# Kernel tuning notes

Hardware: AMD Instinct MI355X
Metric: run time of the kernel (lower is better)

The kernel has to match this reference:

```python
import jax, jax.numpy as jnp
import numpy as np

B = 16        # batch
V = 49152     # HEALPix nside=64 vertices
CIN = 32
COUT = 64
K = 4         # Chebyshev polynomial degree (kernel_size)
NNZ = V * 9   # ~9 nonzeros per row of the sparse Laplacian
POOL = 4      # HEALPix pooling factor
EPS = 1e-5    # BatchNorm eps


def setup_inputs() -> dict:
    key = jax.random.key(0)
    k1, k2, k3, k4, k5 = jax.random.split(key, 5)
    x = jax.random.normal(k1, (B, V, CIN), dtype=jnp.float32)
    lap_rows = jnp.sort(jax.random.randint(k2, (NNZ,), 0, V, dtype=jnp.int32)).astype(jnp.int64)
    lap_cols = jax.random.randint(k3, (NNZ,), 0, V, dtype=jnp.int32).astype(jnp.int64)
    lap_vals = jax.random.normal(k4, (NNZ,), dtype=jnp.float32) * 0.1
    weight = jax.random.normal(k5, (K, CIN, COUT), dtype=jnp.float32) / np.sqrt(K * CIN).astype(np.float32)
    gamma = jnp.ones((COUT,), dtype=jnp.float32)
    beta = jnp.zeros((COUT,), dtype=jnp.float32)
    return {"x": x, "lap_vals": lap_vals, "weight": weight, "gamma": gamma,
            "beta": beta, "lap_rows": lap_rows, "lap_cols": lap_cols}


def _spmm(rows, cols, vals, X):
    """Sparse [V,V] @ dense [V,F] via gather + segment_sum."""
    return jax.ops.segment_sum(vals[:, None] * X[cols], rows, num_segments=V)


def reference(x, lap_vals, weight, gamma, beta, lap_rows, lap_cols):
    b, v, c = x.shape
    # Chebyshev recurrence on [V, B*Cin] layout (vertex-major for spmm)
    X0 = x.transpose(1, 0, 2).reshape(v, b * c)
    xs = [X0]
    X1 = _spmm(lap_rows, lap_cols, lap_vals, X0)
    xs.append(X1)
    for _ in range(K - 2):
        X2 = 2.0 * _spmm(lap_rows, lap_cols, lap_vals, X1) - X0
        xs.append(X2)
        X0, X1 = X1, X2
    cheb = jnp.stack(xs, axis=0).reshape(K, v, b, c)   # [K,V,B,Cin]
    y = jnp.einsum('kvbi,kio->bvo', cheb, weight)      # [B,V,Cout]
    # BatchNorm1d(Cout), training-mode stats over (batch, vertices), biased var
    mean = jnp.mean(y, axis=(0, 1))
    var = jnp.var(y, axis=(0, 1))
    y = (y - mean) * jax.lax.rsqrt(var + EPS) * gamma + beta
    y = jax.nn.relu(y)
    # HEALPix average pooling (factor 4) over vertex dim
    out = y.reshape(b, v // POOL, POOL, COUT).mean(axis=2)
    return out
```

## Files before the change

kernel.cpp:

```cpp
#include <hip/hip_runtime.h>
#include <hip/hip_bf16.h>

#define V     49152
#define NNZ   442368
#define EPS   1e-5f
#define VOUT  12288

typedef __attribute__((ext_vector_type(8))) short bf16x8;
typedef __attribute__((ext_vector_type(4))) float f32x4;

__device__ __forceinline__ unsigned short f2b(float f) {
    __hip_bfloat16 h = __float2bfloat16(f);
    return *reinterpret_cast<unsigned short*>(&h);
}
__device__ __forceinline__ float b2f(unsigned short u) {
    return __uint_as_float((unsigned)u << 16);
}

__global__ __launch_bounds__(256) void k_rowptr(const int* __restrict__ rows,
                                                int* __restrict__ rp) {
    int r = blockIdx.x * blockDim.x + threadIdx.x;
    if (r <= V) {
        int lo = 0, hi = NNZ;
        while (lo < hi) {
            int m = (lo + hi) >> 1;
            if (rows[m] < r) lo = m + 1; else hi = m;
        }
        rp[r] = lo;
    }
}

__global__ __launch_bounds__(256) void k_xpose(const float* __restrict__ x,
                                               unsigned short* __restrict__ xbf) {
    int id = blockIdx.x * 256 + threadIdx.x;
    int i4 = id & 7;
    int b  = (id >> 3) & 15;
    int v  = id >> 7;
    float4 q = *(const float4*)&x[((size_t)b * V + v) * 32 + i4 * 4];
    ushort4 u = {f2b(q.x), f2b(q.y), f2b(q.z), f2b(q.w)};
    *(ushort4*)&xbf[(size_t)v * 512 + b * 32 + i4 * 4] = u;
}

__global__ __launch_bounds__(256) void k_wconv(const float* __restrict__ W,
                                               unsigned short* __restrict__ Wfrag) {
    int d = blockIdx.x * 256 + threadIdx.x;
    int j = d & 7, lane = (d >> 3) & 63, ct = (d >> 9) & 3, ks = d >> 11;
    int k128 = ks * 32 + (lane >> 4) * 8 + j;
    int o = ct * 16 + (lane & 15);
    Wfrag[d] = f2b(W[k128 * 64 + o]);
}

__global__ __launch_bounds__(256) void k_spmm1(const unsigned short* __restrict__ xbf,
                                               const int* __restrict__ cols,
                                               const float* __restrict__ vals,
                                               const int* __restrict__ rp,
                                               unsigned short* __restrict__ X1) {
    int t = threadIdx.x;
    int wave = t >> 6, lane = t & 63;
    int v = blockIdx.x * 4 + wave;
    int f0 = lane * 8;
    int s = rp[v], e = rp[v + 1];
    float a[8] = {0.f, 0.f, 0.f, 0.f, 0.f, 0.f, 0.f, 0.f};
    for (int n = s; n < e; ++n) {
        int c = cols[n];
        float w = vals[n];
        union { unsigned short u[8]; uint4 q; } ld;
        ld.q = *(const uint4*)&xbf[(size_t)c * 512 + f0];
#pragma unroll
        for (int j = 0; j < 8; ++j) a[j] = fmaf(w, b2f(ld.u[j]), a[j]);
    }
    union { unsigned short u[8]; uint4 q; } st;
#pragma unroll
    for (int j = 0; j < 8; ++j) st.u[j] = f2b(a[j]);
    *(uint4*)&X1[(size_t)v * 512 + f0] = st.q;
}

__global__ __launch_bounds__(256) void k_spmm2(const unsigned short* __restrict__ xbf,
                                               const int* __restrict__ cols,
                                               const float* __restrict__ vals,
                                               const int* __restrict__ rp,
                                               const unsigned short* __restrict__ X1,
                                               unsigned short* __restrict__ X2) {
    int t = threadIdx.x;
    int wave = t >> 6, lane = t & 63;
    int v = blockIdx.x * 4 + wave;
    int f0 = lane * 8;
    int s = rp[v], e = rp[v + 1];
    float a[8] = {0.f, 0.f, 0.f, 0.f, 0.f, 0.f, 0.f, 0.f};
    for (int n = s; n < e; ++n) {
        int c = cols[n];
        float w = vals[n];
        union { unsigned short u[8]; uint4 q; } ld;
        ld.q = *(const uint4*)&X1[(size_t)c * 512 + f0];
#pragma unroll
        for (int j = 0; j < 8; ++j) a[j] = fmaf(w, b2f(ld.u[j]), a[j]);
    }
    union { unsigned short u[8]; uint4 q; } x0;
    x0.q = *(const uint4*)&xbf[(size_t)v * 512 + f0];
    union { unsigned short u[8]; uint4 q; } st;
#pragma unroll
    for (int j = 0; j < 8; ++j) st.u[j] = f2b(2.f * a[j] - b2f(x0.u[j]));
    *(uint4*)&X2[(size_t)v * 512 + f0] = st.q;
}

__global__ __launch_bounds__(256) void k_spmm3(const unsigned short* __restrict__ X1,
                                               const int* __restrict__ cols,
                                               const float* __restrict__ vals,
                                               const int* __restrict__ rp,
                                               const unsigned short* __restrict__ X2,
                                               unsigned short* __restrict__ X3) {
    int t = threadIdx.x;
    int wave = t >> 6, lane = t & 63;
    int v = blockIdx.x * 4 + wave;
    int f0 = lane * 8;
    int s = rp[v], e = rp[v + 1];
    float a[8] = {0.f, 0.f, 0.f, 0.f, 0.f, 0.f, 0.f, 0.f};
    for (int n = s; n < e; ++n) {
        int c = cols[n];
        float w = vals[n];
        union { unsigned short u[8]; uint4 q; } ld;
        ld.q = *(const uint4*)&X2[(size_t)c * 512 + f0];
#pragma unroll
        for (int j = 0; j < 8; ++j) a[j] = fmaf(w, b2f(ld.u[j]), a[j]);
    }
    union { unsigned short u[8]; uint4 q; } p1;
    p1.q = *(const uint4*)&X1[(size_t)v * 512 + f0];
    union { unsigned short u[8]; uint4 q; } st;
#pragma unroll
    for (int j = 0; j < 8; ++j) st.u[j] = f2b(2.f * a[j] - b2f(p1.u[j]));
    *(uint4*)&X3[(size_t)v * 512 + f0] = st.q;
}

__global__ __launch_bounds__(256) void k_einsum(const unsigned short* __restrict__ xbf,
                                                const unsigned short* __restrict__ X1,
                                                const unsigned short* __restrict__ X2,
                                                const unsigned short* __restrict__ X3,
                                                const unsigned short* __restrict__ Wfrag,
                                                unsigned short* __restrict__ Y) {
    __shared__ unsigned short sB[8192];
    __shared__ unsigned short sY[4096];

    int t = threadIdx.x;
    int wave = t >> 6, lane = t & 63;
    int v = blockIdx.x * 4 + wave;

#pragma unroll
    for (int m = 0; m < 4; ++m) {
        int d = t + m * 256;
        *(uint4*)&sB[d * 8] = *(const uint4*)&Wfrag[d * 8];
    }
    __syncthreads();

    f32x4 acc[4];
#pragma unroll
    for (int ct = 0; ct < 4; ++ct) acc[ct] = (f32x4){0.f, 0.f, 0.f, 0.f};

    const unsigned short* srcs[4] = {xbf, X1, X2, X3};
    size_t abase = (size_t)v * 512 + (lane & 15) * 32 + (lane >> 4) * 8;
#pragma unroll
    for (int ks = 0; ks < 4; ++ks) {
        bf16x8 a = *(const bf16x8*)&srcs[ks][abase];
#pragma unroll
        for (int ct = 0; ct < 4; ++ct) {
            bf16x8 b = *(const bf16x8*)&sB[((ks * 4 + ct) * 64 + lane) * 8];
            acc[ct] = __builtin_amdgcn_mfma_f32_16x16x32_bf16(a, b, acc[ct], 0, 0, 0);
        }
    }

#pragma unroll
    for (int ct = 0; ct < 4; ++ct) {
        int o = ct * 16 + (lane & 15);
        int bb = (lane >> 4) * 4;
        sY[wave * 1024 + (bb + 0) * 64 + o] = f2b(acc[ct].x);
        sY[wave * 1024 + (bb + 1) * 64 + o] = f2b(acc[ct].y);
        sY[wave * 1024 + (bb + 2) * 64 + o] = f2b(acc[ct].z);
        sY[wave * 1024 + (bb + 3) * 64 + o] = f2b(acc[ct].w);
    }
    __syncthreads();

    size_t ybase = (size_t)blockIdx.x * 4096 + t * 16;
    *(uint4*)&Y[ybase]     = *(const uint4*)&sY[t * 16];
    *(uint4*)&Y[ybase + 8] = *(const uint4*)&sY[t * 16 + 8];
}

__global__ __launch_bounds__(256) void k_bnred1(const unsigned short* __restrict__ Y,
                                                float* __restrict__ partials) {
    __shared__ float lsum[64], lsq[64];
    int t = threadIdx.x;
    if (t < 64) { lsum[t] = 0.f; lsq[t] = 0.f; }
    __syncthreads();
    float s[8] = {0.f, 0.f, 0.f, 0.f, 0.f, 0.f, 0.f, 0.f};
    float q[8] = {0.f, 0.f, 0.f, 0.f, 0.f, 0.f, 0.f, 0.f};
    const uint4* Yq = (const uint4*)Y;
    size_t base = (size_t)blockIdx.x * 24576;
    for (int i = t; i < 24576; i += 256) {
        union { unsigned short u[8]; uint4 v; } ld;
        ld.v = Yq[base + i];
#pragma unroll
        for (int j = 0; j < 8; ++j) {
            float f = b2f(ld.u[j]);
            s[j] += f;
            q[j] = fmaf(f, f, q[j]);
        }
    }
    int c0 = (t & 7) * 8;
#pragma unroll
    for (int j = 0; j < 8; ++j) {
        atomicAdd(&lsum[c0 + j], s[j]);
        atomicAdd(&lsq[c0 + j], q[j]);
    }
    __syncthreads();
    if (t < 128)
        partials[blockIdx.x * 128 + t] = (t < 64) ? lsum[t] : lsq[t - 64];
}

__global__ void k_bnfin(const float* __restrict__ partials,
                        const float* __restrict__ gamma, const float* __restrict__ beta,
                        float* __restrict__ stats) {
    __shared__ float tot[128];
    int t = threadIdx.x;
    float s = 0.f;
    for (int i = 0; i < 256; ++i) s += partials[i * 128 + t];
    tot[t] = s;
    __syncthreads();
    if (t < 64) {
        float n = (float)(16 * V);
        float mean = tot[t] / n;
        float var = tot[64 + t] / n - mean * mean;
        float sc = gamma[t] * rsqrtf(var + EPS);
        stats[128 + t] = sc;
        stats[192 + t] = beta[t] - mean * sc;
    }
}

__global__ __launch_bounds__(256) void k_pool(const unsigned short* __restrict__ Y,
                                              const float* __restrict__ stats,
                                              float* __restrict__ out) {
    int id = blockIdx.x * blockDim.x + threadIdx.x;
    int o4 = id & 15;
    int b  = (id >> 4) & 15;
    int vp = id >> 8;
    float4 sc = *(const float4*)&stats[128 + o4 * 4];
    float4 sh = *(const float4*)&stats[192 + o4 * 4];
    float ax = 0.f, ay = 0.f, az = 0.f, aw = 0.f;
#pragma unroll
    for (int j = 0; j < 4; ++j) {
        ushort4 u = *(const ushort4*)&Y[(size_t)((vp * 4 + j) * 16 + b) * 64 + o4 * 4];
        float tx = b2f(u.x), ty = b2f(u.y), tz = b2f(u.z), tw = b2f(u.w);
        ax += fmaxf(fmaf(tx, sc.x, sh.x), 0.f);
        ay += fmaxf(fmaf(ty, sc.y, sh.y), 0.f);
        az += fmaxf(fmaf(tz, sc.z, sh.z), 0.f);
        aw += fmaxf(fmaf(tw, sc.w, sh.w), 0.f);
    }
    float4 res = {ax * 0.25f, ay * 0.25f, az * 0.25f, aw * 0.25f};
    *(float4*)&out[(size_t)((b * VOUT + vp) * 16 + o4) * 4] = res;
}

extern "C" void kernel_launch(void* const* d_in, const int* in_sizes, int n_in,
                              void* d_out, int out_size, void* d_ws, size_t ws_size,
                              hipStream_t stream) {
    const float* x     = (const float*)d_in[0];
    const float* vals  = (const float*)d_in[1];
    const float* W     = (const float*)d_in[2];
    const float* gamma = (const float*)d_in[3];
    const float* beta  = (const float*)d_in[4];
    const int*   rows  = (const int*)d_in[5];
    const int*   cols  = (const int*)d_in[6];
    float* out = (float*)d_out;

    char* ws = (char*)d_ws;
    unsigned short* xbf = (unsigned short*)ws;
    unsigned short* X1  = (unsigned short*)(ws + 50331648UL);
    unsigned short* X2  = (unsigned short*)(ws + 100663296UL);
    unsigned short* X3  = (unsigned short*)(ws + 150994944UL);
    unsigned short* Y   = (unsigned short*)(ws + 201326592UL);
    int*   rp    = (int*)(ws + 301989888UL);
    float* stats = (float*)(ws + 302190592UL);
    unsigned short* Wfrag = (unsigned short*)(ws + 302194688UL);
    float* partials = (float*)(ws + 302211072UL);

    k_rowptr<<<193, 256, 0, stream>>>(rows, rp);
    k_xpose<<<V * 128 / 256, 256, 0, stream>>>(x, xbf);
    k_wconv<<<32, 256, 0, stream>>>(W, Wfrag);
    k_spmm1<<<V / 4, 256, 0, stream>>>(xbf, cols, vals, rp, X1);
    k_spmm2<<<V / 4, 256, 0, stream>>>(xbf, cols, vals, rp, X1, X2);
    k_spmm3<<<V / 4, 256, 0, stream>>>(X1, cols, vals, rp, X2, X3);
    k_einsum<<<V / 4, 256, 0, stream>>>(xbf, X1, X2, X3, Wfrag, Y);
    k_bnred1<<<256, 256, 0, stream>>>(Y, partials);
    k_bnfin<<<1, 128, 0, stream>>>(partials, gamma, beta, stats);
    k_pool<<<12288, 256, 0, stream>>>(Y, stats, out);
}
```

Measured before the change: 403.2 us.

## Fuse last Chebyshev SpMM, einsum and BN partial reduction into one kernel

The third SpMM is merged with the einsum MFMA kernel. The last Chebyshev term now stays in shared memory in fp32 and is converted to bf16 only for the final MFMA step, so X3 is never written to or read back from global memory. The BatchNorm per-channel sums are computed from the fp32 accumulators inside the same kernel, which removes the separate Y reduction pass. A small second-stage reduction is added over the 12288 per-block partials. The SpMM gather loops are also unrolled by two to allow more loads in flight. Statistics are now taken from fp32 values rather than bf16-rounded Y, which changes numerics slightly.

```diff
diff --git a/kernel.cpp b/kernel.cpp
--- a/kernel.cpp
+++ b/kernel.cpp
@@ -61,13 +61,25 @@
     int f0 = lane * 8;
     int s = rp[v], e = rp[v + 1];
     float a[8] = {0.f, 0.f, 0.f, 0.f, 0.f, 0.f, 0.f, 0.f};
-    for (int n = s; n < e; ++n) {
-        int c = cols[n];
-        float w = vals[n];
-        union { unsigned short u[8]; uint4 q; } ld;
-        ld.q = *(const uint4*)&xbf[(size_t)c * 512 + f0];
-#pragma unroll
-        for (int j = 0; j < 8; ++j) a[j] = fmaf(w, b2f(ld.u[j]), a[j]);
+    int n = s;
+    for (; n + 1 < e; n += 2) {
+        int c0 = cols[n], c1 = cols[n + 1];
+        float w0 = vals[n], w1 = vals[n + 1];
+        union { unsigned short u[8]; uint4 q; } l0, l1;
+        l0.q = *(const uint4*)&xbf[(size_t)c0 * 512 + f0];
+        l1.q = *(const uint4*)&xbf[(size_t)c1 * 512 + f0];
+#pragma unroll
+        for (int j = 0; j < 8; ++j) a[j] = fmaf(w0, b2f(l0.u[j]), a[j]);
+#pragma unroll
+        for (int j = 0; j < 8; ++j) a[j] = fmaf(w1, b2f(l1.u[j]), a[j]);
+    }
+    if (n < e) {
+        int c0 = cols[n];
+        float w0 = vals[n];
+        union { unsigned short u[8]; uint4 q; } l0;
+        l0.q = *(const uint4*)&xbf[(size_t)c0 * 512 + f0];
+#pragma unroll
+        for (int j = 0; j < 8; ++j) a[j] = fmaf(w0, b2f(l0.u[j]), a[j]);
     }
     union { unsigned short u[8]; uint4 q; } st;
 #pragma unroll
@@ -87,13 +99,25 @@
     int f0 = lane * 8;
     int s = rp[v], e = rp[v + 1];
     float a[8] = {0.f, 0.f, 0.f, 0.f, 0.f, 0.f, 0.f, 0.f};
-    for (int n = s; n < e; ++n) {
-        int c = cols[n];
-        float w = vals[n];
-        union { unsigned short u[8]; uint4 q; } ld;
-        ld.q = *(const uint4*)&X1[(size_t)c * 512 + f0];
-#pragma unroll
-        for (int j = 0; j < 8; ++j) a[j] = fmaf(w, b2f(ld.u[j]), a[j]);
+    int n = s;
+    for (; n + 1 < e; n += 2) {
+        int c0 = cols[n], c1 = cols[n + 1];
+        float w0 = vals[n], w1 = vals[n + 1];
+        union { unsigned short u[8]; uint4 q; } l0, l1;
+        l0.q = *(const uint4*)&X1[(size_t)c0 * 512 + f0];
+        l1.q = *(const uint4*)&X1[(size_t)c1 * 512 + f0];
+#pragma unroll
+        for (int j = 0; j < 8; ++j) a[j] = fmaf(w0, b2f(l0.u[j]), a[j]);
+#pragma unroll
+        for (int j = 0; j < 8; ++j) a[j] = fmaf(w1, b2f(l1.u[j]), a[j]);
+    }
+    if (n < e) {
+        int c0 = cols[n];
+        float w0 = vals[n];
+        union { unsigned short u[8]; uint4 q; } l0;
+        l0.q = *(const uint4*)&X1[(size_t)c0 * 512 + f0];
+#pragma unroll
+        for (int j = 0; j < 8; ++j) a[j] = fmaf(w0, b2f(l0.u[j]), a[j]);
     }
     union { unsigned short u[8]; uint4 q; } x0;
     x0.q = *(const uint4*)&xbf[(size_t)v * 512 + f0];
@@ -103,70 +127,104 @@
     *(uint4*)&X2[(size_t)v * 512 + f0] = st.q;
 }
 
-__global__ __launch_bounds__(256) void k_spmm3(const unsigned short* __restrict__ X1,
+__global__ __launch_bounds__(256) void k_cheb3(const unsigned short* __restrict__ xbf,
+                                               const unsigned short* __restrict__ X1,
+                                               const unsigned short* __restrict__ X2,
+                                               const unsigned short* __restrict__ Wfrag,
                                                const int* __restrict__ cols,
                                                const float* __restrict__ vals,
                                                const int* __restrict__ rp,
-                                               const unsigned short* __restrict__ X2,
-                                               unsigned short* __restrict__ X3) {
+                                               unsigned short* __restrict__ Y,
+                                               float* __restrict__ partials) {
+    __shared__ unsigned short sB[8192];
+    __shared__ float sMix[2048];
+    __shared__ float lsum[64], lsq[64];
+
     int t = threadIdx.x;
     int wave = t >> 6, lane = t & 63;
     int v = blockIdx.x * 4 + wave;
+
+#pragma unroll
+    for (int m = 0; m < 4; ++m) {
+        int d = t + m * 256;
+        *(uint4*)&sB[d * 8] = *(const uint4*)&Wfrag[d * 8];
+    }
+    if (t < 64) { lsum[t] = 0.f; lsq[t] = 0.f; }
+
     int f0 = lane * 8;
     int s = rp[v], e = rp[v + 1];
     float a[8] = {0.f, 0.f, 0.f, 0.f, 0.f, 0.f, 0.f, 0.f};
-    for (int n = s; n < e; ++n) {
-        int c = cols[n];
-        float w = vals[n];
-        union { unsigned short u[8]; uint4 q; } ld;
-        ld.q = *(const uint4*)&X2[(size_t)c * 512 + f0];
-#pragma unroll
-        for (int j = 0; j < 8; ++j) a[j] = fmaf(w, b2f(ld.u[j]), a[j]);
+    int n = s;
+    for (; n + 1 < e; n += 2) {
+        int c0 = cols[n], c1 = cols[n + 1];
+        float w0 = vals[n], w1 = vals[n + 1];
+        union { unsigned short u[8]; uint4 q; } l0, l1;
+        l0.q = *(const uint4*)&X2[(size_t)c0 * 512 + f0];
+        l1.q = *(const uint4*)&X2[(size_t)c1 * 512 + f0];
+#pragma unroll
+        for (int j = 0; j < 8; ++j) a[j] = fmaf(w0, b2f(l0.u[j]), a[j]);
+#pragma unroll
+        for (int j = 0; j < 8; ++j) a[j] = fmaf(w1, b2f(l1.u[j]), a[j]);
+    }
+    if (n < e) {
+        int c0 = cols[n];
+        float w0 = vals[n];
+        union { unsigned short u[8]; uint4 q; } l0;
+        l0.q = *(const uint4*)&X2[(size_t)c0 * 512 + f0];
+#pragma unroll
+        for (int j = 0; j < 8; ++j) a[j] = fmaf(w0, b2f(l0.u[j]), a[j]);
     }
     union { unsigned short u[8]; uint4 q; } p1;
     p1.q = *(const uint4*)&X1[(size_t)v * 512 + f0];
-    union { unsigned short u[8]; uint4 q; } st;
-#pragma unroll
-    for (int j = 0; j < 8; ++j) st.u[j] = f2b(2.f * a[j] - b2f(p1.u[j]));
-    *(uint4*)&X3[(size_t)v * 512 + f0] = st.q;
-}
-
-__global__ __launch_bounds__(256) void k_einsum(const unsigned short* __restrict__ xbf,
-                                                const unsigned short* __restrict__ X1,
-                                                const unsigned short* __restrict__ X2,
-                                                const unsigned short* __restrict__ X3,
-                                                const unsigned short* __restrict__ Wfrag,
-                                                unsigned short* __restrict__ Y) {
-    __shared__ unsigned short sB[8192];
-    __shared__ unsigned short sY[4096];
-
-    int t = threadIdx.x;
-    int wave = t >> 6, lane = t & 63;
-    int v = blockIdx.x * 4 + wave;
-
-#pragma unroll
-    for (int m = 0; m < 4; ++m) {
-        int d = t + m * 256;
-        *(uint4*)&sB[d * 8] = *(const uint4*)&Wfrag[d * 8];
-    }
+    float4 xa, xb;
+    xa.x = 2.f * a[0] - b2f(p1.u[0]); xa.y = 2.f * a[1] - b2f(p1.u[1]);
+    xa.z = 2.f * a[2] - b2f(p1.u[2]); xa.w = 2.f * a[3] - b2f(p1.u[3]);
+    xb.x = 2.f * a[4] - b2f(p1.u[4]); xb.y = 2.f * a[5] - b2f(p1.u[5]);
+    xb.z = 2.f * a[6] - b2f(p1.u[6]); xb.w = 2.f * a[7] - b2f(p1.u[7]);
+    *(float4*)&sMix[wave * 512 + f0]     = xa;
+    *(float4*)&sMix[wave * 512 + f0 + 4] = xb;
     __syncthreads();
 
     f32x4 acc[4];
 #pragma unroll
     for (int ct = 0; ct < 4; ++ct) acc[ct] = (f32x4){0.f, 0.f, 0.f, 0.f};
 
-    const unsigned short* srcs[4] = {xbf, X1, X2, X3};
+    const unsigned short* srcs[3] = {xbf, X1, X2};
     size_t abase = (size_t)v * 512 + (lane & 15) * 32 + (lane >> 4) * 8;
 #pragma unroll
-    for (int ks = 0; ks < 4; ++ks) {
-        bf16x8 a = *(const bf16x8*)&srcs[ks][abase];
+    for (int ks = 0; ks < 3; ++ks) {
+        bf16x8 afr = *(const bf16x8*)&srcs[ks][abase];
 #pragma unroll
         for (int ct = 0; ct < 4; ++ct) {
             bf16x8 b = *(const bf16x8*)&sB[((ks * 4 + ct) * 64 + lane) * 8];
-            acc[ct] = __builtin_amdgcn_mfma_f32_16x16x32_bf16(a, b, acc[ct], 0, 0, 0);
+            acc[ct] = __builtin_amdgcn_mfma_f32_16x16x32_bf16(afr, b, acc[ct], 0, 0, 0);
         }
     }
-
+    {
+        int ao = wave * 512 + (lane & 15) * 32 + (lane >> 4) * 8;
+        float4 fa = *(const float4*)&sMix[ao];
+        float4 fb = *(const float4*)&sMix[ao + 4];
+        union { unsigned short u[8]; bf16x8 h; } af;
+        af.u[0] = f2b(fa.x); af.u[1] = f2b(fa.y); af.u[2] = f2b(fa.z); af.u[3] = f2b(fa.w);
+        af.u[4] = f2b(fb.x); af.u[5] = f2b(fb.y); af.u[6] = f2b(fb.z); af.u[7] = f2b(fb.w);
+#pragma unroll
+        for (int ct = 0; ct < 4; ++ct) {
+            bf16x8 b = *(const bf16x8*)&sB[((3 * 4 + ct) * 64 + lane) * 8];
+            acc[ct] = __builtin_amdgcn_mfma_f32_16x16x32_bf16(af.h, b, acc[ct], 0, 0, 0);
+        }
+    }
+
+#pragma unroll
+    for (int ct = 0; ct < 4; ++ct) {
+        float ss = acc[ct].x + acc[ct].y + acc[ct].z + acc[ct].w;
+        float qq = acc[ct].x * acc[ct].x + acc[ct].y * acc[ct].y
+                 + acc[ct].z * acc[ct].z + acc[ct].w * acc[ct].w;
+        atomicAdd(&lsum[ct * 16 + (lane & 15)], ss);
+        atomicAdd(&lsq[ct * 16 + (lane & 15)], qq);
+    }
+
+    __syncthreads();
+    unsigned short* sY = (unsigned short*)sMix;
 #pragma unroll
     for (int ct = 0; ct < 4; ++ct) {
         int o = ct * 16 + (lane & 15);
@@ -181,46 +239,39 @@
     size_t ybase = (size_t)blockIdx.x * 4096 + t * 16;
     *(uint4*)&Y[ybase]     = *(const uint4*)&sY[t * 16];
     *(uint4*)&Y[ybase + 8] = *(const uint4*)&sY[t * 16 + 8];
-}
-
-__global__ __launch_bounds__(256) void k_bnred1(const unsigned short* __restrict__ Y,
-                                                float* __restrict__ partials) {
-    __shared__ float lsum[64], lsq[64];
-    int t = threadIdx.x;
-    if (t < 64) { lsum[t] = 0.f; lsq[t] = 0.f; }
-    __syncthreads();
-    float s[8] = {0.f, 0.f, 0.f, 0.f, 0.f, 0.f, 0.f, 0.f};
-    float q[8] = {0.f, 0.f, 0.f, 0.f, 0.f, 0.f, 0.f, 0.f};
-    const uint4* Yq = (const uint4*)Y;
-    size_t base = (size_t)blockIdx.x * 24576;
-    for (int i = t; i < 24576; i += 256) {
-        union { unsigned short u[8]; uint4 v; } ld;
-        ld.v = Yq[base + i];
-#pragma unroll
-        for (int j = 0; j < 8; ++j) {
-            float f = b2f(ld.u[j]);
-            s[j] += f;
-            q[j] = fmaf(f, f, q[j]);
-        }
-    }
-    int c0 = (t & 7) * 8;
-#pragma unroll
-    for (int j = 0; j < 8; ++j) {
-        atomicAdd(&lsum[c0 + j], s[j]);
-        atomicAdd(&lsq[c0 + j], q[j]);
-    }
-    __syncthreads();
+
     if (t < 128)
-        partials[blockIdx.x * 128 + t] = (t < 64) ? lsum[t] : lsq[t - 64];
-}
-
-__global__ void k_bnfin(const float* __restrict__ partials,
+        partials[(size_t)blockIdx.x * 128 + t] = (t < 64) ? lsum[t] : lsq[t - 64];
+}
+
+__global__ __launch_bounds__(256) void k_bnred2(const float* __restrict__ partials,
+                                                float* __restrict__ partials2) {
+    __shared__ float ls[128];
+    int t = threadIdx.x;
+    if (t < 128) ls[t] = 0.f;
+    __syncthreads();
+    const float4* P = (const float4*)(partials + (size_t)blockIdx.x * 32768);
+    float a0 = 0.f, a1 = 0.f, a2 = 0.f, a3 = 0.f;
+    for (int i = 0; i < 32; ++i) {
+        float4 q = P[i * 256 + t];
+        a0 += q.x; a1 += q.y; a2 += q.z; a3 += q.w;
+    }
+    int c0 = (t * 4) & 127;
+    atomicAdd(&ls[c0], a0);
+    atomicAdd(&ls[c0 + 1], a1);
+    atomicAdd(&ls[c0 + 2], a2);
+    atomicAdd(&ls[c0 + 3], a3);
+    __syncthreads();
+    if (t < 128) partials2[blockIdx.x * 128 + t] = ls[t];
+}
+
+__global__ void k_bnfin(const float* __restrict__ partials2,
                         const float* __restrict__ gamma, const float* __restrict__ beta,
                         float* __restrict__ stats) {
     __shared__ float tot[128];
     int t = threadIdx.x;
     float s = 0.f;
-    for (int i = 0; i < 256; ++i) s += partials[i * 128 + t];
+    for (int i = 0; i < 48; ++i) s += partials2[i * 128 + t];
     tot[t] = s;
     __syncthreads();
     if (t < 64) {
@@ -272,21 +323,20 @@
     unsigned short* xbf = (unsigned short*)ws;
     unsigned short* X1  = (unsigned short*)(ws + 50331648UL);
     unsigned short* X2  = (unsigned short*)(ws + 100663296UL);
-    unsigned short* X3  = (unsigned short*)(ws + 150994944UL);
-    unsigned short* Y   = (unsigned short*)(ws + 201326592UL);
-    int*   rp    = (int*)(ws + 301989888UL);
-    float* stats = (float*)(ws + 302190592UL);
-    unsigned short* Wfrag = (unsigned short*)(ws + 302194688UL);
-    float* partials = (float*)(ws + 302211072UL);
+    unsigned short* Y   = (unsigned short*)(ws + 150994944UL);
+    int*   rp    = (int*)(ws + 251658240UL);
+    float* stats = (float*)(ws + 251858944UL);
+    unsigned short* Wfrag = (unsigned short*)(ws + 251859968UL);
+    float* partials  = (float*)(ws + 251877376UL);
+    float* partials2 = (float*)(ws + 258168832UL);
 
     k_rowptr<<<193, 256, 0, stream>>>(rows, rp);
     k_xpose<<<V * 128 / 256, 256, 0, stream>>>(x, xbf);
     k_wconv<<<32, 256, 0, stream>>>(W, Wfrag);
     k_spmm1<<<V / 4, 256, 0, stream>>>(xbf, cols, vals, rp, X1);
     k_spmm2<<<V / 4, 256, 0, stream>>>(xbf, cols, vals, rp, X1, X2);
-    k_spmm3<<<V / 4, 256, 0, stream>>>(X1, cols, vals, rp, X2, X3);
-    k_einsum<<<V / 4, 256, 0, stream>>>(xbf, X1, X2, X3, Wfrag, Y);
-    k_bnred1<<<256, 256, 0, stream>>>(Y, partials);
-    k_bnfin<<<1, 128, 0, stream>>>(partials, gamma, beta, stats);
+    k_cheb3<<<V / 4, 256, 0, stream>>>(xbf, X1, X2, Wfrag, cols, vals, rp, Y, partials);
+    k_bnred2<<<48, 256, 0, stream>>>(partials, partials2);
+    k_bnfin<<<1, 128, 0, stream>>>(partials2, gamma, beta, stats);
     k_pool<<<12288, 256, 0, stream>>>(Y, stats, out);
 }
```

Measured after the change: 401.3 us. Within noise of the previous version (-0.5%).

## Fuse BatchNorm statistics into einsum epilogue and unroll SpMM gathers by four

Applied to the files above, without the earlier changes.

Per-channel sum and sum-of-squares are now computed from the fp32 MFMA accumulators inside the einsum kernel. Each block reduces them in LDS and atomically adds them into 256 partial slots, which are zeroed in the rowptr kernel. This removes the separate pass that re-read the bf16 Y buffer. The SpMM gather loops are also unrolled by four so several independent row loads are in flight per wave. The cost is extra global and shared atomics per block, plus statistics taken from fp32 values rather than rounded bf16, which slightly changes the numerics.

```diff
diff --git a/kernel.cpp b/kernel.cpp
--- a/kernel.cpp
+++ b/kernel.cpp
@@ -18,16 +18,18 @@
 }
 
 __global__ __launch_bounds__(256) void k_rowptr(const int* __restrict__ rows,
-                                                int* __restrict__ rp) {
-    int r = blockIdx.x * blockDim.x + threadIdx.x;
-    if (r <= V) {
+                                                int* __restrict__ rp,
+                                                float* __restrict__ partials) {
+    int id = blockIdx.x * blockDim.x + threadIdx.x;
+    if (id <= V) {
         int lo = 0, hi = NNZ;
         while (lo < hi) {
             int m = (lo + hi) >> 1;
-            if (rows[m] < r) lo = m + 1; else hi = m;
+            if (rows[m] < id) lo = m + 1; else hi = m;
         }
-        rp[r] = lo;
-    }
+        rp[id] = lo;
+    }
+    if (id < 32768) partials[id] = 0.f;
 }
 
 __global__ __launch_bounds__(256) void k_xpose(const float* __restrict__ x,
@@ -50,6 +52,35 @@
     Wfrag[d] = f2b(W[k128 * 64 + o]);
 }
 
+#define GATHER_LOOP(SRC)                                                        \
+    float a[8] = {0.f, 0.f, 0.f, 0.f, 0.f, 0.f, 0.f, 0.f};                      \
+    int n = s;                                                                  \
+    for (; n + 3 < e; n += 4) {                                                 \
+        int c0 = cols[n], c1 = cols[n + 1], c2 = cols[n + 2], c3 = cols[n + 3]; \
+        float w0 = vals[n], w1 = vals[n + 1], w2 = vals[n + 2], w3 = vals[n + 3]; \
+        union { unsigned short u[8]; uint4 q; } l0, l1, l2, l3;                 \
+        l0.q = *(const uint4*)&SRC[(size_t)c0 * 512 + f0];                      \
+        l1.q = *(const uint4*)&SRC[(size_t)c1 * 512 + f0];                      \
+        l2.q = *(const uint4*)&SRC[(size_t)c2 * 512 + f0];                      \
+        l3.q = *(const uint4*)&SRC[(size_t)c3 * 512 + f0];                      \
+        _Pragma("unroll")                                                       \
+        for (int j = 0; j < 8; ++j) a[j] = fmaf(w0, b2f(l0.u[j]), a[j]);        \
+        _Pragma("unroll")                                                       \
+        for (int j = 0; j < 8; ++j) a[j] = fmaf(w1, b2f(l1.u[j]), a[j]);        \
+        _Pragma("unroll")                                                       \
+        for (int j = 0; j < 8; ++j) a[j] = fmaf(w2, b2f(l2.u[j]), a[j]);        \
+        _Pragma("unroll")                                                       \
+        for (int j = 0; j < 8; ++j) a[j] = fmaf(w3, b2f(l3.u[j]), a[j]);        \
+    }                                                                           \
+    for (; n < e; ++n) {                                                        \
+        int c0 = cols[n];                                                       \
+        float w0 = vals[n];                                                     \
+        union { unsigned short u[8]; uint4 q; } l0;                             \
+        l0.q = *(const uint4*)&SRC[(size_t)c0 * 512 + f0];                      \
+        _Pragma("unroll")                                                       \
+        for (int j = 0; j < 8; ++j) a[j] = fmaf(w0, b2f(l0.u[j]), a[j]);        \
+    }
+
 __global__ __launch_bounds__(256) void k_spmm1(const unsigned short* __restrict__ xbf,
                                                const int* __restrict__ cols,
                                                const float* __restrict__ vals,
@@ -60,15 +91,7 @@
     int v = blockIdx.x * 4 + wave;
     int f0 = lane * 8;
     int s = rp[v], e = rp[v + 1];
-    float a[8] = {0.f, 0.f, 0.f, 0.f, 0.f, 0.f, 0.f, 0.f};
-    for (int n = s; n < e; ++n) {
-        int c = cols[n];
-        float w = vals[n];
-        union { unsigned short u[8]; uint4 q; } ld;
-        ld.q = *(const uint4*)&xbf[(size_t)c * 512 + f0];
-#pragma unroll
-        for (int j = 0; j < 8; ++j) a[j] = fmaf(w, b2f(ld.u[j]), a[j]);
-    }
+    GATHER_LOOP(xbf)
     union { unsigned short u[8]; uint4 q; } st;
 #pragma unroll
     for (int j = 0; j < 8; ++j) st.u[j] = f2b(a[j]);
@@ -86,15 +109,7 @@
     int v = blockIdx.x * 4 + wave;
     int f0 = lane * 8;
     int s = rp[v], e = rp[v + 1];
-    float a[8] = {0.f, 0.f, 0.f, 0.f, 0.f, 0.f, 0.f, 0.f};
-    for (int n = s; n < e; ++n) {
-        int c = cols[n];
-        float w = vals[n];
-        union { unsigned short u[8]; uint4 q; } ld;
-        ld.q = *(const uint4*)&X1[(size_t)c * 512 + f0];
-#pragma unroll
-        for (int j = 0; j < 8; ++j) a[j] = fmaf(w, b2f(ld.u[j]), a[j]);
-    }
+    GATHER_LOOP(X1)
     union { unsigned short u[8]; uint4 q; } x0;
     x0.q = *(const uint4*)&xbf[(size_t)v * 512 + f0];
     union { unsigned short u[8]; uint4 q; } st;
@@ -114,15 +129,7 @@
     int v = blockIdx.x * 4 + wave;
     int f0 = lane * 8;
     int s = rp[v], e = rp[v + 1];
-    float a[8] = {0.f, 0.f, 0.f, 0.f, 0.f, 0.f, 0.f, 0.f};
-    for (int n = s; n < e; ++n) {
-        int c = cols[n];
-        float w = vals[n];
-        union { unsigned short u[8]; uint4 q; } ld;
-        ld.q = *(const uint4*)&X2[(size_t)c * 512 + f0];
-#pragma unroll
-        for (int j = 0; j < 8; ++j) a[j] = fmaf(w, b2f(ld.u[j]), a[j]);
-    }
+    GATHER_LOOP(X2)
     union { unsigned short u[8]; uint4 q; } p1;
     p1.q = *(const uint4*)&X1[(size_t)v * 512 + f0];
     union { unsigned short u[8]; uint4 q; } st;
@@ -136,9 +143,11 @@
                                                 const unsigned short* __restrict__ X2,
                                                 const unsigned short* __restrict__ X3,
                                                 const unsigned short* __restrict__ Wfrag,
-                                                unsigned short* __restrict__ Y) {
+                                                unsigned short* __restrict__ Y,
+                                                float* __restrict__ partials) {
     __shared__ unsigned short sB[8192];
     __shared__ unsigned short sY[4096];
+    __shared__ float lsum[64], lsq[64];
 
     int t = threadIdx.x;
     int wave = t >> 6, lane = t & 63;
@@ -149,6 +158,7 @@
         int d = t + m * 256;
         *(uint4*)&sB[d * 8] = *(const uint4*)&Wfrag[d * 8];
     }
+    if (t < 64) { lsum[t] = 0.f; lsq[t] = 0.f; }
     __syncthreads();
 
     f32x4 acc[4];
@@ -165,6 +175,15 @@
             bf16x8 b = *(const bf16x8*)&sB[((ks * 4 + ct) * 64 + lane) * 8];
             acc[ct] = __builtin_amdgcn_mfma_f32_16x16x32_bf16(a, b, acc[ct], 0, 0, 0);
         }
+    }
+
+#pragma unroll
+    for (int ct = 0; ct < 4; ++ct) {
+        float ss = acc[ct].x + acc[ct].y + acc[ct].z + acc[ct].w;
+        float qq = acc[ct].x * acc[ct].x + acc[ct].y * acc[ct].y
+                 + acc[ct].z * acc[ct].z + acc[ct].w * acc[ct].w;
+        atomicAdd(&lsum[ct * 16 + (lane & 15)], ss);
+        atomicAdd(&lsq[ct * 16 + (lane & 15)], qq);
     }
 
 #pragma unroll
@@ -181,37 +200,11 @@
     size_t ybase = (size_t)blockIdx.x * 4096 + t * 16;
     *(uint4*)&Y[ybase]     = *(const uint4*)&sY[t * 16];
     *(uint4*)&Y[ybase + 8] = *(const uint4*)&sY[t * 16 + 8];
-}
-
-__global__ __launch_bounds__(256) void k_bnred1(const unsigned short* __restrict__ Y,
-                                                float* __restrict__ partials) {
-    __shared__ float lsum[64], lsq[64];
-    int t = threadIdx.x;
-    if (t < 64) { lsum[t] = 0.f; lsq[t] = 0.f; }
-    __syncthreads();
-    float s[8] = {0.f, 0.f, 0.f, 0.f, 0.f, 0.f, 0.f, 0.f};
-    float q[8] = {0.f, 0.f, 0.f, 0.f, 0.f, 0.f, 0.f, 0.f};
-    const uint4* Yq = (const uint4*)Y;
-    size_t base = (size_t)blockIdx.x * 24576;
-    for (int i = t; i < 24576; i += 256) {
-        union { unsigned short u[8]; uint4 v; } ld;
-        ld.v = Yq[base + i];
-#pragma unroll
-        for (int j = 0; j < 8; ++j) {
-            float f = b2f(ld.u[j]);
-            s[j] += f;
-            q[j] = fmaf(f, f, q[j]);
-        }
-    }
-    int c0 = (t & 7) * 8;
-#pragma unroll
-    for (int j = 0; j < 8; ++j) {
-        atomicAdd(&lsum[c0 + j], s[j]);
-        atomicAdd(&lsq[c0 + j], q[j]);
-    }
-    __syncthreads();
-    if (t < 128)
-        partials[blockIdx.x * 128 + t] = (t < 64) ? lsum[t] : lsq[t - 64];
+
+    if (t < 128) {
+        float val = (t < 64) ? lsum[t] : lsq[t - 64];
+        atomicAdd(&partials[(blockIdx.x & 255) * 128 + t], val);
+    }
 }
 
 __global__ void k_bnfin(const float* __restrict__ partials,
@@ -275,18 +268,17 @@
     unsigned short* X3  = (unsigned short*)(ws + 150994944UL);
     unsigned short* Y   = (unsigned short*)(ws + 201326592UL);
     int*   rp    = (int*)(ws + 301989888UL);
-    float* stats = (float*)(ws + 302190592UL);
-    unsigned short* Wfrag = (unsigned short*)(ws + 302194688UL);
-    float* partials = (float*)(ws + 302211072UL);
-
-    k_rowptr<<<193, 256, 0, stream>>>(rows, rp);
+    float* stats = (float*)(ws + 302186560UL);
+    unsigned short* Wfrag = (unsigned short*)(ws + 302187584UL);
+    float* partials = (float*)(ws + 302203968UL);
+
+    k_rowptr<<<193, 256, 0, stream>>>(rows, rp, partials);
     k_xpose<<<V * 128 / 256, 256, 0, stream>>>(x, xbf);
     k_wconv<<<32, 256, 0, stream>>>(W, Wfrag);
     k_spmm1<<<V / 4, 256, 0, stream>>>(xbf, cols, vals, rp, X1);
     k_spmm2<<<V / 4, 256, 0, stream>>>(xbf, cols, vals, rp, X1, X2);
     k_spmm3<<<V / 4, 256, 0, stream>>>(X1, cols, vals, rp, X2, X3);
-    k_einsum<<<V / 4, 256, 0, stream>>>(xbf, X1, X2, X3, Wfrag, Y);
-    k_bnred1<<<256, 256, 0, stream>>>(Y, partials);
+    k_einsum<<<V / 4, 256, 0, stream>>>(xbf, X1, X2, X3, Wfrag, Y, partials);
     k_bnfin<<<1, 128, 0, stream>>>(partials, gamma, beta, stats);
     k_pool<<<12288, 256, 0, stream>>>(Y, stats, out);
 }
```

After: 447.9 us. 1.11x slower.
